# Kernel tuning notes

Hardware: AMD Instinct MI355X
Metric: run time of the kernel (lower is better)

Reference implementation:

```python
import jax, jax.numpy as jnp
import numpy as np

N_HEADS = 16

def setup_inputs() -> dict:
    key = jax.random.key(0)
    qkv = jax.random.normal(key, (4, 3072, 2048), dtype=jnp.float32)
    return {"qkv": qkv}

def reference(qkv) -> jnp.ndarray:
    bs, width, length = qkv.shape
    ch = width // (3 * N_HEADS)
    # [bs*H, 3*ch, T] -> split into q, k, v each [bs*H, ch, T]
    qkv_r = qkv.reshape(bs * N_HEADS, 3 * ch, length)
    q, k, v = qkv_r[:, :ch], qkv_r[:, ch:2 * ch], qkv_r[:, 2 * ch:]
    scale = 1.0 / jnp.sqrt(jnp.sqrt(jnp.float32(ch)))
    # scores: [bs*H, T, T]
    weight = jnp.einsum('bct,bcs->bts', q * scale, k * scale)
    weight = jax.nn.softmax(weight.astype(jnp.float32), axis=-1).astype(weight.dtype)
    a = jnp.einsum('bts,bcs->bct', weight, v)  # [bs*H, ch, T]
    return a.reshape(bs, N_HEADS * ch, length)
```

## Files before the change

### kernel.cpp

```cpp
#include <hip/hip_runtime.h>

namespace {

constexpr int D  = 64;
constexpr int T  = 2048;
constexpr int NT = T / 64;
constexpr float SCL = 0.125f * 1.44269504088896340736f;

constexpr size_t QP_OFF  = (size_t)64 * 32 * 8192;
constexpr size_t WS_NEED = ((size_t)64 * 32 * 8192 + (size_t)64 * 32 * 4096) * 2;

typedef __bf16 bf16x8 __attribute__((ext_vector_type(8)));
typedef float  f32x4  __attribute__((ext_vector_type(4)));
typedef unsigned short u16x4 __attribute__((ext_vector_type(4)));
typedef unsigned short u16x8 __attribute__((ext_vector_type(8)));
typedef unsigned int   u32x2 __attribute__((ext_vector_type(2)));
typedef unsigned int   u32x4 __attribute__((ext_vector_type(4)));

__device__ inline unsigned short f2bf(float f) {
    unsigned int u = __builtin_bit_cast(unsigned int, f);
    u += 0x7FFFu + ((u >> 16) & 1u);
    return (unsigned short)(u >> 16);
}

__device__ inline unsigned int pkbf(float a, float b) {
#if __has_builtin(__builtin_amdgcn_cvt_pk_bf16_f32)
    auto r = __builtin_amdgcn_cvt_pk_bf16_f32(a, b);
    static_assert(sizeof(r) == 4, "cvt_pk_bf16 size");
    return __builtin_bit_cast(unsigned int, r);
#else
    return (unsigned int)f2bf(a) | ((unsigned int)f2bf(b) << 16);
#endif
}

__device__ inline int frag_off(int row, int c0) {
    int g = (c0 >> 3) ^ ((row >> 1) & 7);
    return row * 64 + g * 8;
}

__device__ inline void async_cp16(const void* g, void* l) {
    __builtin_amdgcn_global_load_lds(
        (const __attribute__((address_space(1))) unsigned int*)g,
        (__attribute__((address_space(3))) unsigned int*)l, 16, 0, 0);
}

__global__ __launch_bounds__(256)
void prepass(const float* __restrict__ qkv, unsigned short* __restrict__ ws) {
    const int tile = blockIdx.x, h = blockIdx.y, z = blockIdx.z;
    const int tid = threadIdx.x;
    const float* src = qkv + (size_t)h * 3 * D * T + (size_t)z * D * T + tile * 64;
    __shared__ unsigned short L[4096];

    if (z == 2) {
        unsigned short* dst = ws + (size_t)(h * 32 + tile) * 8192 + 4096;
        const int c = tid >> 2, pg = tid & 3;
        const int slot = pg ^ ((c >> 2) & 3);
        #pragma unroll
        for (int b = 0; b < 2; b++) {
            f32x4 a0 = *(const f32x4*)(src + (size_t)c * T + b * 32 + pg * 4);
            f32x4 a1 = *(const f32x4*)(src + (size_t)c * T + b * 32 + 16 + pg * 4);
            u16x8 wv = { f2bf(a0[0]), f2bf(a0[1]), f2bf(a0[2]), f2bf(a0[3]),
                         f2bf(a1[0]), f2bf(a1[1]), f2bf(a1[2]), f2bf(a1[3]) };
            *(u16x8*)(dst + b * 2048 + c * 32 + slot * 8) = wv;
        }
    } else {
        const float m = (z == 0) ? SCL : 1.0f;
        const int c0 = (tid >> 4) * 4, s4 = tid & 15;
        float fr[4][4];
        #pragma unroll
        for (int r = 0; r < 4; r++)
            *(f32x4*)fr[r] = *(const f32x4*)(src + (size_t)(c0 + r) * T + s4 * 4);
        #pragma unroll
        for (int j = 0; j < 4; j++) {
            int trow = s4 * 4 + j;
            u16x4 wv = { f2bf(fr[0][j] * m), f2bf(fr[1][j] * m),
                         f2bf(fr[2][j] * m), f2bf(fr[3][j] * m) };
            *(u16x4*)(L + frag_off(trow, c0) + (c0 & 7)) = wv;
        }
        __syncthreads();
        unsigned short* dst = (z == 0)
            ? ws + QP_OFF + (size_t)(h * 32 + tile) * 4096
            : ws + (size_t)(h * 32 + tile) * 8192;
        #pragma unroll
        for (int i = 0; i < 2; i++)
            *(u16x8*)(dst + tid * 16 + i * 8) = *(const u16x8*)(L + tid * 16 + i * 8);
    }
}


#define STAGE(J, SB)                                                         \
  { const char* g = kvb + (size_t)(J) * 16384;                               \
    char* lk = lbase + (SB) * 16384;                                         \
    async_cp16(g,         lk);                                               \
    async_cp16(g + 4096,  lk + 4096);                                        \
    async_cp16(g + 8192,  lk + 8192);                                        \
    async_cp16(g + 12288, lk + 12288); }

#define BODY(KT, B, SB, DO_STAGE, WAITIMM)                                   \
  {                                                                          \
    __builtin_amdgcn_s_waitcnt(WAITIMM);         \
    __builtin_amdgcn_s_barrier();          \
    __builtin_amdgcn_sched_barrier(0);          \
    if (DO_STAGE) STAGE((KT) + 2, SB)     \
    __builtin_amdgcn_s_setprio(1);                                           \
    _Pragma("unroll")                                                        \
    for (int j = 0; j < 2; j++) {         \
      const char* kq0 = sbuf + (B) * 16384 + (2 * j) * 2048;                 \
      const char* kq1 = kq0 + 2048;                                          \
      const char* vbj = sbuf + (B) * 16384 + 8192 + j * 4096;                \
      bf16x8 aK00 = *(const bf16x8*)(kq0 + aK0o);                            \
      bf16x8 aK01 = *(const bf16x8*)(kq0 + aK1o);                            \
      bf16x8 aK10 = *(const bf16x8*)(kq1 + aK0o);                            \
      bf16x8 aK11 = *(const bf16x8*)(kq1 + aK1o);                            \
      bf16x8 aV0 = *(const bf16x8*)(vbj + aVo);                              \
      bf16x8 aV1 = *(const bf16x8*)(vbj + aVo + 1024);                       \
      bf16x8 aV2 = *(const bf16x8*)(vbj + aVo + 2048);                       \
      bf16x8 aV3 = *(const bf16x8*)(vbj + aVo + 3072);                       \
      _Pragma("unroll")                                                      \
      for (int st = 0; st < 2; st++) {                                       \
        f32x4 s0 = __builtin_amdgcn_mfma_f32_16x16x32_bf16(                  \
            aK00, bQ[st][0], ZF, 0, 0, 0);                                   \
        s0 = __builtin_amdgcn_mfma_f32_16x16x32_bf16(                        \
            aK01, bQ[st][1], s0, 0, 0, 0);                                   \
        f32x4 s1 = __builtin_amdgcn_mfma_f32_16x16x32_bf16(                  \
            aK10, bQ[st][0], ZF, 0, 0, 0);                                   \
        s1 = __builtin_amdgcn_mfma_f32_16x16x32_bf16(                        \
            aK11, bQ[st][1], s1, 0, 0, 0);                                   \
        float p0 = __builtin_amdgcn_exp2f(s0[0]);                            \
        float p1 = __builtin_amdgcn_exp2f(s0[1]);                            \
        float p2 = __builtin_amdgcn_exp2f(s0[2]);                            \
        float p3 = __builtin_amdgcn_exp2f(s0[3]);                            \
        float q0 = __builtin_amdgcn_exp2f(s1[0]);                            \
        float q1 = __builtin_amdgcn_exp2f(s1[1]);                            \
        float q2 = __builtin_amdgcn_exp2f(s1[2]);                            \
        float q3 = __builtin_amdgcn_exp2f(s1[3]);                            \
        l_acc[st] += ((p0 + p1) + (p2 + p3)) + ((q0 + q1) + (q2 + q3));      \
        u32x4 pk = { pkbf(p0, p1), pkbf(p2, p3),                             \
                     pkbf(q0, q1), pkbf(q2, q3) };                           \
        bf16x8 bPP = __builtin_bit_cast(bf16x8, pk);                         \
        acc_o[st][0] = __builtin_amdgcn_mfma_f32_16x16x32_bf16(              \
            aV0, bPP, acc_o[st][0], 0, 0, 0);                                \
        acc_o[st][1] = __builtin_amdgcn_mfma_f32_16x16x32_bf16(              \
            aV1, bPP, acc_o[st][1], 0, 0, 0);                                \
        acc_o[st][2] = __builtin_amdgcn_mfma_f32_16x16x32_bf16(              \
            aV2, bPP, acc_o[st][2], 0, 0, 0);                                \
        acc_o[st][3] = __builtin_amdgcn_mfma_f32_16x16x32_bf16(              \
            aV3, bPP, acc_o[st][3], 0, 0, 0);                                \
      }                                                                      \
    }                                                                        \
    __builtin_amdgcn_s_setprio(0);                                           \
  }

__global__ __launch_bounds__(256, 3)
void attn_main(const unsigned short* __restrict__ ws, float* __restrict__ out) {
    const int h  = blockIdx.x;
    const int qt = blockIdx.y;
    const int t0 = qt * 128;
    const int tid  = threadIdx.x;
    const int lane = tid & 63;
    const int w    = tid >> 6;
    const int ln   = lane & 15, q4 = lane >> 4;

    __shared__ char sbuf[49152];
    char* lbase = sbuf + w * 1024;

    const int aK0o = 2 * frag_off(ln, q4 * 8);
    const int aK1o = 2 * frag_off(ln, 32 + q4 * 8);
    const int aVo  = 64 * ln + ((q4 ^ ((ln >> 2) & 3)) * 16);

    const unsigned short* qtile = ws + QP_OFF + (size_t)(h * 32 + qt * 2) * 4096;
    bf16x8 bQ[2][2];
    #pragma unroll
    for (int st = 0; st < 2; st++) {
        bQ[st][0] = *(const bf16x8*)(qtile + st * 4096 + frag_off(16 * w + ln, q4 * 8));
        bQ[st][1] = *(const bf16x8*)(qtile + st * 4096 + frag_off(16 * w + ln, 32 + q4 * 8));
    }

    const char* kvb = (const char*)ws + (size_t)(h * 32) * 16384
                      + w * 1024 + lane * 16;
    STAGE(0, 0)
    STAGE(1, 1)

    const f32x4 ZF = {0.f, 0.f, 0.f, 0.f};
    f32x4 acc_o[2][4];
    #pragma unroll
    for (int st = 0; st < 2; st++)
        #pragma unroll
        for (int ci = 0; ci < 4; ci++) acc_o[st][ci] = ZF;
    float l_acc[2] = {0.f, 0.f};

    #pragma unroll 1
    for (int m = 0; m < 10; m++) {
        BODY(3 * m,     0, 2, 1, 0x0F74)
        BODY(3 * m + 1, 1, 0, 1, 0x0F74)
        BODY(3 * m + 2, 2, 1, 1, 0x0F74)
    }
    BODY(30, 0, 0, 0, 0x0F74)
    BODY(31, 1, 0, 0, 0x0F70)

    #pragma unroll
    for (int st = 0; st < 2; st++) {
        float sl = l_acc[st];
        sl += __shfl_xor(sl, 16, 64);
        sl += __shfl_xor(sl, 32, 64);
        const float linv = 1.0f / sl;
        float* ob = out + (size_t)h * D * T + t0 + st * 64 + 16 * w + ln;
        #pragma unroll
        for (int ci = 0; ci < 4; ci++)
            #pragma unroll
            for (int rr = 0; rr < 4; rr++)
                ob[(size_t)(16 * ci + q4 * 4 + rr) * T] = acc_o[st][ci][rr] * linv;
    }
}

__device__ inline bf16x8 frag8(const unsigned short* p, int row, int c0) {
    return *(const bf16x8*)(p + frag_off(row, c0));
}

__global__ __launch_bounds__(256)
void attn_fallback(const float* __restrict__ qkv, float* __restrict__ out) {
    const int h     = blockIdx.y;
    const int t0    = blockIdx.x * 64;
    const int tid   = threadIdx.x;
    const int lane  = tid & 63;
    const int strip = tid >> 6;
    const int ln    = lane & 15;
    const int q4    = lane >> 4;

    __shared__ unsigned short Qs[64 * D];
    __shared__ unsigned short Ks[64 * D];
    __shared__ unsigned short Vs[D * 64];
    __shared__ unsigned short Pss[64 * 64];
    __shared__ float l_lds[64];

    const float* qb = qkv + (size_t)h * 3 * D * T;
    const float* kb = qb + (size_t)D * T;
    const float* vb = qb + (size_t)(2 * D) * T;
    const int s4 = tid & 15;
    const int c0 = (tid >> 4) * 4;
    {
        float fr[4][4];
        #pragma unroll
        for (int r = 0; r < 4; r++)
            *(f32x4*)fr[r] = *(const f32x4*)(qb + (size_t)(c0 + r) * T + t0 + s4 * 4);
        #pragma unroll
        for (int j = 0; j < 4; j++) {
            int trow = s4 * 4 + j;
            u16x4 wv = { f2bf(fr[0][j]), f2bf(fr[1][j]), f2bf(fr[2][j]), f2bf(fr[3][j]) };
            *(u16x4*)(Qs + frag_off(trow, c0) + (c0 & 7)) = wv;
        }
    }
    __syncthreads();
    const int arow = strip * 16 + ln;
    const int kg   = q4 * 8;
    const bf16x8 aq0 = frag8(Qs, arow, kg);
    const bf16x8 aq1 = frag8(Qs, arow, 32 + kg);
    f32x4 acc_o[4];
    #pragma unroll
    for (int m = 0; m < 4; m++) acc_o[m] = (f32x4){0.f, 0.f, 0.f, 0.f};
    float l_acc[4] = {0.f, 0.f, 0.f, 0.f};
    constexpr float S2 = 0.125f * 1.44269504088896340736f;
    for (int kt = 0; kt < NT; kt++) {
        const int s0 = kt * 64;
        float kr[4][4], vr[4][4];
        #pragma unroll
        for (int r = 0; r < 4; r++)
            *(f32x4*)kr[r] = *(const f32x4*)(kb + (size_t)(c0 + r) * T + s0 + s4 * 4);
        #pragma unroll
        for (int r = 0; r < 4; r++)
            *(f32x4*)vr[r] = *(const f32x4*)(vb + (size_t)(c0 + r) * T + s0 + s4 * 4);
        __syncthreads();
        #pragma unroll
        for (int j = 0; j < 4; j++) {
            int srow = s4 * 4 + j;
            u16x4 wk = { f2bf(kr[0][j]), f2bf(kr[1][j]), f2bf(kr[2][j]), f2bf(kr[3][j]) };
            *(u16x4*)(Ks + frag_off(srow, c0) + (c0 & 7)) = wk;
        }
        #pragma unroll
        for (int r = 0; r < 4; r++) {
            int row = c0 + r, cc = s4 * 4;
            u16x4 wv = { f2bf(vr[r][0]), f2bf(vr[r][1]), f2bf(vr[r][2]), f2bf(vr[r][3]) };
            *(u16x4*)(Vs + frag_off(row, cc) + (cc & 7)) = wv;
        }
        __syncthreads();
        f32x4 accs[4];
        #pragma unroll
        for (int ns = 0; ns < 4; ns++) {
            bf16x8 b0 = frag8(Ks, ns * 16 + ln, kg);
            bf16x8 b1 = frag8(Ks, ns * 16 + ln, 32 + kg);
            f32x4 z = {0.f, 0.f, 0.f, 0.f};
            z = __builtin_amdgcn_mfma_f32_16x16x32_bf16(aq0, b0, z, 0, 0, 0);
            z = __builtin_amdgcn_mfma_f32_16x16x32_bf16(aq1, b1, z, 0, 0, 0);
            accs[ns] = z;
        }
        #pragma unroll
        for (int ns = 0; ns < 4; ns++) {
            int scol = ns * 16 + ln;
            #pragma unroll
            for (int r = 0; r < 4; r++) {
                float p = __builtin_amdgcn_exp2f(accs[ns][r] * S2);
                l_acc[r] += p;
                int trow = strip * 16 + q4 * 4 + r;
                int g = ((scol >> 3) ^ ((trow >> 1) & 7));
                Pss[trow * 64 + g * 8 + (scol & 7)] = f2bf(p);
            }
        }
        bf16x8 bp0 = frag8(Pss, arow, kg);
        bf16x8 bp1 = frag8(Pss, arow, 32 + kg);
        #pragma unroll
        for (int ms = 0; ms < 4; ms++) {
            bf16x8 av0 = frag8(Vs, ms * 16 + ln, kg);
            bf16x8 av1 = frag8(Vs, ms * 16 + ln, 32 + kg);
            acc_o[ms] = __builtin_amdgcn_mfma_f32_16x16x32_bf16(av0, bp0, acc_o[ms], 0, 0, 0);
            acc_o[ms] = __builtin_amdgcn_mfma_f32_16x16x32_bf16(av1, bp1, acc_o[ms], 0, 0, 0);
        }
    }
    #pragma unroll
    for (int r = 0; r < 4; r++) {
        float s = l_acc[r];
        s += __shfl_xor(s, 1, 64);
        s += __shfl_xor(s, 2, 64);
        s += __shfl_xor(s, 4, 64);
        s += __shfl_xor(s, 8, 64);
        if (ln == 0) l_lds[strip * 16 + q4 * 4 + r] = s;
    }
    const float linv = 1.0f / l_lds[strip * 16 + ln];
    const int tg = t0 + strip * 16 + ln;
    float* ob = out + (size_t)h * D * T;
    #pragma unroll
    for (int ms = 0; ms < 4; ms++)
        #pragma unroll
        for (int r = 0; r < 4; r++) {
            int c = ms * 16 + q4 * 4 + r;
            ob[(size_t)c * T + tg] = acc_o[ms][r] * linv;
        }
}

}

extern "C" void kernel_launch(void* const* d_in, const int* in_sizes, int n_in,
                              void* d_out, int out_size, void* d_ws, size_t ws_size,
                              hipStream_t stream) {
    const float* qkv = (const float*)d_in[0];
    float* out = (float*)d_out;
    if (ws_size >= WS_NEED) {
        prepass<<<dim3(32, 64, 3), 256, 0, stream>>>(qkv, (unsigned short*)d_ws);
        attn_main<<<dim3(64, 16), 256, 0, stream>>>((const unsigned short*)d_ws, out);
    } else {
        attn_fallback<<<dim3(32, 64), 256, 0, stream>>>(qkv, out);
    }
}
```

Measured before the change: 238.9 us.

## Merge prepass z-blocks into one block and re-swizzle V tile layout

The prepass now processes Q, K and V for a tile in one block, looping over Q and K and then writing V, instead of launching three z-slices. The V workspace layout changes from two 32-column halves to full 64-element rows with an XOR swizzle over 8 slots, and the attention kernel's V fragment addressing is updated to match. This cuts the number of prepass blocks and may change LDS bank behaviour for V reads. The cost is fewer, longer prepass blocks with an extra barrier.

```diff
diff --git a/kernel.cpp b/kernel.cpp
--- a/kernel.cpp
+++ b/kernel.cpp
@@ -46,30 +46,20 @@
 
 __global__ __launch_bounds__(256)
 void prepass(const float* __restrict__ qkv, unsigned short* __restrict__ ws) {
-    const int tile = blockIdx.x, h = blockIdx.y, z = blockIdx.z;
+    const int tile = blockIdx.x, h = blockIdx.y;
     const int tid = threadIdx.x;
-    const float* src = qkv + (size_t)h * 3 * D * T + (size_t)z * D * T + tile * 64;
     __shared__ unsigned short L[4096];
-
-    if (z == 2) {
-        unsigned short* dst = ws + (size_t)(h * 32 + tile) * 8192 + 4096;
-        const int c = tid >> 2, pg = tid & 3;
-        const int slot = pg ^ ((c >> 2) & 3);
-        #pragma unroll
-        for (int b = 0; b < 2; b++) {
-            f32x4 a0 = *(const f32x4*)(src + (size_t)c * T + b * 32 + pg * 4);
-            f32x4 a1 = *(const f32x4*)(src + (size_t)c * T + b * 32 + 16 + pg * 4);
-            u16x8 wv = { f2bf(a0[0]), f2bf(a0[1]), f2bf(a0[2]), f2bf(a0[3]),
-                         f2bf(a1[0]), f2bf(a1[1]), f2bf(a1[2]), f2bf(a1[3]) };
-            *(u16x8*)(dst + b * 2048 + c * 32 + slot * 8) = wv;
-        }
-    } else {
+    const int c0 = (tid >> 4) * 4, s4 = tid & 15;
+
+    #pragma unroll
+    for (int z = 0; z < 2; z++) {
+        const float* src = qkv + (size_t)h * 3 * D * T + (size_t)z * D * T + tile * 64;
         const float m = (z == 0) ? SCL : 1.0f;
-        const int c0 = (tid >> 4) * 4, s4 = tid & 15;
         float fr[4][4];
         #pragma unroll
         for (int r = 0; r < 4; r++)
             *(f32x4*)fr[r] = *(const f32x4*)(src + (size_t)(c0 + r) * T + s4 * 4);
+        if (z) __syncthreads();
         #pragma unroll
         for (int j = 0; j < 4; j++) {
             int trow = s4 * 4 + j;
@@ -84,6 +74,21 @@
         #pragma unroll
         for (int i = 0; i < 2; i++)
             *(u16x8*)(dst + tid * 16 + i * 8) = *(const u16x8*)(L + tid * 16 + i * 8);
+    }
+
+    {
+        const float* src = qkv + (size_t)h * 3 * D * T + (size_t)(2) * D * T + tile * 64;
+        unsigned short* dst = ws + (size_t)(h * 32 + tile) * 8192 + 4096;
+        const int c = tid >> 2, pg = tid & 3;
+        const int swz = (c >> 1) & 7;
+        #pragma unroll
+        for (int j = 0; j < 2; j++) {
+            f32x4 a0 = *(const f32x4*)(src + (size_t)c * T + j * 32 + pg * 4);
+            f32x4 a1 = *(const f32x4*)(src + (size_t)c * T + j * 32 + 16 + pg * 4);
+            u16x8 wv = { f2bf(a0[0]), f2bf(a0[1]), f2bf(a0[2]), f2bf(a0[3]),
+                         f2bf(a1[0]), f2bf(a1[1]), f2bf(a1[2]), f2bf(a1[3]) };
+            *(u16x8*)(dst + c * 64 + ((4 * j + pg) ^ swz) * 8) = wv;
+        }
     }
 }
 
@@ -107,15 +112,16 @@
     for (int j = 0; j < 2; j++) {         \
       const char* kq0 = sbuf + (B) * 16384 + (2 * j) * 2048;                 \
       const char* kq1 = kq0 + 2048;                                          \
-      const char* vbj = sbuf + (B) * 16384 + 8192 + j * 4096;                \
+      const char* vbb = sbuf + (B) * 16384 + 8192;                           \
+      const int av = aVo ^ (j * 64);                                         \
       bf16x8 aK00 = *(const bf16x8*)(kq0 + aK0o);                            \
       bf16x8 aK01 = *(const bf16x8*)(kq0 + aK1o);                            \
       bf16x8 aK10 = *(const bf16x8*)(kq1 + aK0o);                            \
       bf16x8 aK11 = *(const bf16x8*)(kq1 + aK1o);                            \
-      bf16x8 aV0 = *(const bf16x8*)(vbj + aVo);                              \
-      bf16x8 aV1 = *(const bf16x8*)(vbj + aVo + 1024);                       \
-      bf16x8 aV2 = *(const bf16x8*)(vbj + aVo + 2048);                       \
-      bf16x8 aV3 = *(const bf16x8*)(vbj + aVo + 3072);                       \
+      bf16x8 aV0 = *(const bf16x8*)(vbb + av);                               \
+      bf16x8 aV1 = *(const bf16x8*)(vbb + av + 2048);                        \
+      bf16x8 aV2 = *(const bf16x8*)(vbb + av + 4096);                        \
+      bf16x8 aV3 = *(const bf16x8*)(vbb + av + 6144);                        \
       _Pragma("unroll")                                                      \
       for (int st = 0; st < 2; st++) {                                       \
         f32x4 s0 = __builtin_amdgcn_mfma_f32_16x16x32_bf16(                  \
@@ -166,7 +172,7 @@
 
     const int aK0o = 2 * frag_off(ln, q4 * 8);
     const int aK1o = 2 * frag_off(ln, 32 + q4 * 8);
-    const int aVo  = 64 * ln + ((q4 ^ ((ln >> 2) & 3)) * 16);
+    const int aVo  = 128 * ln + 16 * (q4 ^ ((ln >> 1) & 7));
 
     const unsigned short* qtile = ws + QP_OFF + (size_t)(h * 32 + qt * 2) * 4096;
     bf16x8 bQ[2][2];
@@ -344,7 +350,7 @@
     const float* qkv = (const float*)d_in[0];
     float* out = (float*)d_out;
     if (ws_size >= WS_NEED) {
-        prepass<<<dim3(32, 64, 3), 256, 0, stream>>>(qkv, (unsigned short*)d_ws);
+        prepass<<<dim3(32, 64), 256, 0, stream>>>(qkv, (unsigned short*)d_ws);
         attn_main<<<dim3(64, 16), 256, 0, stream>>>((const unsigned short*)d_ws, out);
     } else {
         attn_fallback<<<dim3(32, 64), 256, 0, stream>>>(qkv, out);
```

After: 241.4 us. Within noise of the previous version (+1.1%).
